# Kernel tuning notes

Measured on AMD Instinct MI355X. Metric: run time of the kernel, lower is better.

Reference implementation:

```python
import jax, jax.numpy as jnp
import numpy as np

WEIGHT = 1.0
TEMPERATURE = 1.0
POWER = 2.0
NEG_FILL = -1e9
EPS = 1e-8


def _cos_sim_matrix(x):
    # row-normalize then GEMM: equivalent to pairwise F.cosine_similarity
    norms = jnp.linalg.norm(x, axis=-1, keepdims=True)
    xn = x / jnp.maximum(norms, EPS)
    return xn @ xn.T  # [N, N]


def setup_inputs() -> dict:
    key = jax.random.key(0)
    k1, k2 = jax.random.split(key)
    model_output = jax.random.normal(k1, (8192, 512), dtype=jnp.float32)
    targets = jax.random.normal(k2, (8192, 768), dtype=jnp.float32)
    return {"model_output": model_output, "targets": targets}


def reference(model_output, targets):
    N = model_output.shape[0]
    eye = jnp.eye(N, dtype=bool)

    sim_o = jnp.where(eye, NEG_FILL, _cos_sim_matrix(model_output))
    sim_t = jnp.where(eye, NEG_FILL, _cos_sim_matrix(targets))

    student_log_probs = jax.nn.log_softmax(sim_o / TEMPERATURE, axis=-1)
    teacher_probs = jax.nn.softmax(sim_t / TEMPERATURE, axis=-1)

    weights = jax.lax.stop_gradient(teacher_probs ** POWER)

    # torch F.kl_div(input=log_p_student, target=p_teacher, reduction='none')
    # = where(target > 0, target * (log(target) - input), 0)
    tp_safe = jnp.where(teacher_probs > 0, teacher_probs, 1.0)
    kl = jnp.where(teacher_probs > 0,
                   teacher_probs * (jnp.log(tp_safe) - student_log_probs),
                   0.0)

    loss = jnp.mean(weights * kl)
    return WEIGHT * loss
```

## Files before the change

kernel.cpp:

```cpp
#include <hip/hip_runtime.h>

#define N    8192
#define DT   768
#define DO   512
#define BM   128
#define BN   128
#define TI   (N / BM)
#define TJ   (N / BN)
#define NTILE (TI * (TI + 1) / 2)
#define NSLOT (2 * TJ)
#define PL    ((size_t)NSLOT * N)
#define NKT   (DT / 32)
#define NKO   (DO / 32)
#define NSTEP (NKT + NKO)

typedef __attribute__((ext_vector_type(8))) short   short8;
typedef __attribute__((ext_vector_type(4))) float   floatx4;

struct alignas(8) us4 { unsigned short x[4]; };

__device__ inline unsigned short f2bf(float x) {
    union { float f; unsigned int u; } v; v.f = x;
    unsigned int r = v.u + 0x7fffu + ((v.u >> 16) & 1u);
    return (unsigned short)(r >> 16);
}
__device__ inline float bf2f(unsigned short u) {
    union { unsigned int u; float f; } v; v.u = ((unsigned int)u) << 16;
    return v.f;
}

__device__ inline void gl2lds16(const unsigned short* g, unsigned short* l) {
    __builtin_amdgcn_global_load_lds(
        (const __attribute__((address_space(1))) unsigned int*)(const void*)g,
        (__attribute__((address_space(3))) unsigned int*)(void*)l,
        16, 0, 0);
}

template <int D>
__device__ inline void stage_tile(const unsigned short* __restrict__ Xi,
                                  const unsigned short* __restrict__ Xj,
                                  unsigned short* sAb, unsigned short* sBb,
                                  int i0, int j0, int k, int t) {
    #pragma unroll
    for (int h = 0; h < 2; ++h) {
        const int idx = t + h * 256;
        const int r   = idx >> 2;
        const int cs  = ((idx & 3) ^ ((r >> 1) & 3)) << 3;
        gl2lds16(Xi + (size_t)(i0 + r) * D + k + cs, &sAb[idx * 8]);
        gl2lds16(Xj + (size_t)(j0 + r) * D + k + cs, &sBb[idx * 8]);
    }
}

__device__ inline void mfma_step(const unsigned short* __restrict__ sAb,
                                 const unsigned short* __restrict__ sBb,
                                 floatx4 (&acc)[4][4],
                                 int wm, int wn, int lr, int lgx) {
    short8 af[4], bf[4];
    #pragma unroll
    for (int mi = 0; mi < 4; ++mi)
        af[mi] = *(const short8*)&sAb[(wm * 64 + mi * 16 + lr) * 32 + (lgx << 3)];
    #pragma unroll
    for (int ni = 0; ni < 4; ++ni)
        bf[ni] = *(const short8*)&sBb[(wn * 64 + ni * 16 + lr) * 32 + (lgx << 3)];
    #pragma unroll
    for (int mi = 0; mi < 4; ++mi)
        #pragma unroll
        for (int ni = 0; ni < 4; ++ni)
            acc[mi][ni] = __builtin_amdgcn_mfma_f32_16x16x32_bf16(
                af[mi], bf[ni], acc[mi][ni], 0, 0, 0);
}

__global__ void norm_kernel(const float* __restrict__ Tg,
                            const float* __restrict__ Mo,
                            unsigned short* __restrict__ Xt,
                            unsigned short* __restrict__ Xo,
                            float* __restrict__ zero_me) {
    if (blockIdx.x == 0 && threadIdx.x == 0) zero_me[0] = 0.0f;
    int bid = blockIdx.x;
    const float* X; unsigned short* Xn; int D;
    if (bid < N / 4) { X = Tg; Xn = Xt; D = DT; }
    else             { bid -= N / 4; X = Mo; Xn = Xo; D = DO; }
    const int row  = bid * 4 + (threadIdx.x >> 6);
    const int lane = threadIdx.x & 63;
    const float* xr = X + (size_t)row * D;
    float ss = 0.0f;
    for (int c = lane * 4; c < D; c += 256) {
        const floatx4 v = *(const floatx4*)(xr + c);
        ss += v[0] * v[0] + v[1] * v[1] + v[2] * v[2] + v[3] * v[3];
    }
    #pragma unroll
    for (int m = 32; m >= 1; m >>= 1) ss += __shfl_xor(ss, m);
    const float scale = 1.0f / fmaxf(sqrtf(ss), 1e-8f);
    unsigned short* outr = Xn + (size_t)row * D;
    for (int c = lane * 4; c < D; c += 256) {
        const floatx4 v = *(const floatx4*)(xr + c);
        us4 o;
        #pragma unroll
        for (int j = 0; j < 4; ++j) o.x[j] = f2bf(v[j] * scale);
        *(us4*)(outr + c) = o;
    }
}

__launch_bounds__(256, 3)
__global__ void fused_kernel(const unsigned short* __restrict__ Xt,
                             const unsigned short* __restrict__ Xo,
                             float* __restrict__ partials,
                             unsigned int* __restrict__ Wws) {
    __shared__ unsigned short sA[3][BM * 32];
    __shared__ unsigned short sB[3][BN * 32];

    const int t    = threadIdx.x;
    const int lane = t & 63;
    const int w    = t >> 6;
    const int wm   = w >> 1, wn = w & 1;
    const int lr   = lane & 15, lg = lane >> 4;
    const int lgx  = lg ^ ((lr >> 1) & 3);

    const int swb = (blockIdx.x & 7) * (NTILE / 8) + (blockIdx.x >> 3);
    int rem = swb, ti = 0;
    while (rem >= TI - ti) { rem -= TI - ti; ++ti; }
    const int tj = ti + rem;
    const bool offdiag = (ti != tj);
    const int i0 = ti * BM, j0 = tj * BN;
    unsigned int* const wt = Wws + (size_t)blockIdx.x * 8192;

    floatx4 acc[4][4];
    #pragma unroll
    for (int a = 0; a < 4; ++a)
        #pragma unroll
        for (int b = 0; b < 4; ++b)
            acc[a][b] = (floatx4){0.0f, 0.0f, 0.0f, 0.0f};

    auto stage_any = [&](int s) {
        unsigned short* a = sA[s % 3];
        unsigned short* b = sB[s % 3];
        if (s < NKT) stage_tile<DT>(Xt, Xt, a, b, i0, j0, s * 32, t);
        else         stage_tile<DO>(Xo, Xo, a, b, i0, j0, (s - NKT) * 32, t);
    };

    stage_any(0);
    stage_any(1);

    for (int kt = 0; kt < NKT; ++kt) {
        stage_any(kt + 2);
        asm volatile("s_waitcnt vmcnt(8)" ::: "memory");
        __builtin_amdgcn_s_barrier();
        asm volatile("" ::: "memory");
        mfma_step(sA[kt % 3], sB[kt % 3], acc, wm, wn, lr, lgx);
        asm volatile("" ::: "memory");
        __builtin_amdgcn_s_barrier();
        asm volatile("" ::: "memory");
    }

    {
        float czt[4], cvv[4], cua[4];
        #pragma unroll
        for (int ni = 0; ni < 4; ++ni) { czt[ni] = 0.0f; cvv[ni] = 0.0f; cua[ni] = 0.0f; }
        #pragma unroll
        for (int mi = 0; mi < 4; ++mi) {
            unsigned int wpk[4][2];
            #pragma unroll
            for (int r = 0; r < 4; ++r) {
                const int row = wm * 64 + mi * 16 + lg * 4 + r;
                const int gi  = i0 + row;
                float zt = 0.0f, vv = 0.0f, ua = 0.0f;
                #pragma unroll
                for (int ni = 0; ni < 4; ++ni) {
                    const int gj = j0 + wn * 64 + ni * 16 + lr;
                    const float a = acc[mi][ni][r];
                    float ea = __expf(a - 1.0f);
                    if (gi == gj) ea = 0.0f;
                    const float e3 = ea * ea * ea;
                    zt += ea; vv += e3; ua += e3 * a;
                    czt[ni] += ea; cvv[ni] += e3; cua[ni] += e3 * a;
                    if ((r & 1) == 0) wpk[ni][r >> 1]  = (unsigned int)f2bf(e3);
                    else              wpk[ni][r >> 1] |= ((unsigned int)f2bf(e3)) << 16;
                }
                #pragma unroll
                for (int m = 8; m >= 1; m >>= 1) {
                    zt += __shfl_xor(zt, m);
                    vv += __shfl_xor(vv, m);
                    ua += __shfl_xor(ua, m);
                }
                if (lr == 0) {
                    const size_t base = (size_t)(tj * 2 + wn) * N + gi;
                    partials[0 * PL + base] = zt;
                    partials[1 * PL + base] = vv;
                    partials[2 * PL + base] = ua;
                }
            }
            #pragma unroll
            for (int ni = 0; ni < 4; ++ni)
                #pragma unroll
                for (int rp = 0; rp < 2; ++rp)
                    wt[(mi * 8 + ni * 2 + rp) * 256 + t] = wpk[ni][rp];
        }
        if (offdiag) {
            #pragma unroll
            for (int ni = 0; ni < 4; ++ni) {
                #pragma unroll
                for (int m = 16; m <= 32; m <<= 1) {
                    czt[ni] += __shfl_xor(czt[ni], m);
                    cvv[ni] += __shfl_xor(cvv[ni], m);
                    cua[ni] += __shfl_xor(cua[ni], m);
                }
            }
            if (lg == 0) {
                #pragma unroll
                for (int ni = 0; ni < 4; ++ni) {
                    const int gj = j0 + wn * 64 + ni * 16 + lr;
                    const size_t base = (size_t)(ti * 2 + wm) * N + gj;
                    partials[0 * PL + base] = czt[ni];
                    partials[1 * PL + base] = cvv[ni];
                    partials[2 * PL + base] = cua[ni];
                }
            }
        }
    }

    #pragma unroll
    for (int a = 0; a < 4; ++a)
        #pragma unroll
        for (int b = 0; b < 4; ++b)
            acc[a][b] = (floatx4){0.0f, 0.0f, 0.0f, 0.0f};

    for (int ko = 0; ko < NKO; ++ko) {
        const int s = NKT + ko;
        if (ko + 2 < NKO) {
            stage_any(s + 2);
            asm volatile("s_waitcnt vmcnt(8)" ::: "memory");
        } else if (ko == NKO - 2) {
            asm volatile("s_waitcnt vmcnt(4)" ::: "memory");
        } else {
            asm volatile("s_waitcnt vmcnt(0)" ::: "memory");
        }
        __builtin_amdgcn_s_barrier();
        asm volatile("" ::: "memory");
        mfma_step(sA[s % 3], sB[s % 3], acc, wm, wn, lr, lgx);
        asm volatile("" ::: "memory");
        if (ko <= NKO - 4) {
            __builtin_amdgcn_s_barrier();
            asm volatile("" ::: "memory");
        }
    }

    {
        unsigned int wld[32];
        #pragma unroll
        for (int pi = 0; pi < 32; ++pi)
            wld[pi] = wt[pi * 256 + t];
        float czo[4], cwb[4];
        #pragma unroll
        for (int ni = 0; ni < 4; ++ni) { czo[ni] = 0.0f; cwb[ni] = 0.0f; }
        #pragma unroll
        for (int mi = 0; mi < 4; ++mi) {
            #pragma unroll
            for (int r = 0; r < 4; ++r) {
                const int row = wm * 64 + mi * 16 + lg * 4 + r;
                const int gi  = i0 + row;
                float zo = 0.0f, wb = 0.0f;
                #pragma unroll
                for (int ni = 0; ni < 4; ++ni) {
                    const int gj = j0 + wn * 64 + ni * 16 + lr;
                    const float b = acc[mi][ni][r];
                    float eb = __expf(b - 1.0f);
                    if (gi == gj) eb = 0.0f;
                    const unsigned int pw = wld[mi * 8 + ni * 2 + (r >> 1)];
                    const float wgt = bf2f((unsigned short)((r & 1) ? (pw >> 16)
                                                                    : (pw & 0xffffu)));
                    zo += eb; wb += wgt * b;
                    czo[ni] += eb; cwb[ni] += wgt * b;
                }
                #pragma unroll
                for (int m = 8; m >= 1; m >>= 1) {
                    zo += __shfl_xor(zo, m);
                    wb += __shfl_xor(wb, m);
                }
                if (lr == 0) {
                    const size_t base = (size_t)(tj * 2 + wn) * N + gi;
                    partials[3 * PL + base] = zo;
                    partials[4 * PL + base] = wb;
                }
            }
        }
        if (offdiag) {
            #pragma unroll
            for (int ni = 0; ni < 4; ++ni) {
                #pragma unroll
                for (int m = 16; m <= 32; m <<= 1) {
                    czo[ni] += __shfl_xor(czo[ni], m);
                    cwb[ni] += __shfl_xor(cwb[ni], m);
                }
            }
            if (lg == 0) {
                #pragma unroll
                for (int ni = 0; ni < 4; ++ni) {
                    const int gj = j0 + wn * 64 + ni * 16 + lr;
                    const size_t base = (size_t)(ti * 2 + wm) * N + gj;
                    partials[3 * PL + base] = czo[ni];
                    partials[4 * PL + base] = cwb[ni];
                }
            }
        }
    }
}

__global__ void reduce_kernel(const float* __restrict__ partials,
                              float* __restrict__ out) {
    __shared__ float sh[5][256];
    const int t    = threadIdx.x;
    const int lane = t & 63;
    const int g    = t >> 6;
    const int i    = blockIdx.x * 64 + lane;
    float s[5] = {0.0f, 0.0f, 0.0f, 0.0f, 0.0f};
    for (int jb = g * (NSLOT / 4); jb < (g + 1) * (NSLOT / 4); ++jb) {
        const size_t base = (size_t)jb * N + i;
        #pragma unroll
        for (int p = 0; p < 5; ++p) s[p] += partials[p * PL + base];
    }
    #pragma unroll
    for (int p = 0; p < 5; ++p) sh[p][t] = s[p];
    __syncthreads();
    if (g == 0) {
        float v[5];
        #pragma unroll
        for (int p = 0; p < 5; ++p)
            v[p] = sh[p][lane] + sh[p][64 + lane] + sh[p][128 + lane] + sh[p][192 + lane];
        float li = (v[2] - v[4] + v[1] * __logf(v[3] / v[0])) / (v[0] * v[0] * v[0]);
        #pragma unroll
        for (int m = 32; m >= 1; m >>= 1) li += __shfl_xor(li, m);
        if (lane == 0)
            atomicAdd(out, li * (1.0f / ((float)N * (float)N)));
    }
}

extern "C" void kernel_launch(void* const* d_in, const int* in_sizes, int n_in,
                              void* d_out, int out_size, void* d_ws, size_t ws_size,
                              hipStream_t stream) {
    (void)in_sizes; (void)n_in; (void)out_size; (void)ws_size;
    const float* mo = (const float*)d_in[0];
    const float* tg = (const float*)d_in[1];
    float* out = (float*)d_out;

    char* ws = (char*)d_ws;
    unsigned short* Xt = (unsigned short*)ws;
    unsigned short* Xo = (unsigned short*)(ws + (size_t)N * DT * 2);
    float* partials    = (float*)(ws + (size_t)N * DT * 2 + (size_t)N * DO * 2);
    unsigned int* Wws  = (unsigned int*)((char*)partials + 5 * PL * sizeof(float));

    norm_kernel<<<2 * (N / 4), 256, 0, stream>>>(tg, mo, Xt, Xo, out);
    fused_kernel<<<NTILE, 256, 0, stream>>>(Xt, Xo, partials, Wws);
    reduce_kernel<<<N / 64, 256, 0, stream>>>(partials, out);
}
```

Baseline: 339.7 us.

## Keep both similarity accumulators in registers and drop weight spill buffer

The fused kernel now holds separate accumulators for the target and output GEMMs and runs a single combined epilogue, so the teacher weights no longer go through a global workspace (bf16 packing, writes and reloads). The K pipeline moves to four LDS stages with one barrier per step, issuing the next load after the barrier. Launch bounds drop from three to two blocks per CU to fit the doubled accumulator registers. The norm kernel caches row values in registers instead of reading each row twice. The trade is lower occupancy against removed global traffic and fewer barriers; the weights now stay in fp32 rather than bf16.

Result: faster. 326.1 us (-4.0%).

```diff
diff --git a/kernel.cpp b/kernel.cpp
--- a/kernel.cpp
+++ b/kernel.cpp
@@ -24,10 +24,6 @@
     unsigned int r = v.u + 0x7fffu + ((v.u >> 16) & 1u);
     return (unsigned short)(r >> 16);
 }
-__device__ inline float bf2f(unsigned short u) {
-    union { unsigned int u; float f; } v; v.u = ((unsigned int)u) << 16;
-    return v.f;
-}
 
 __device__ inline void gl2lds16(const unsigned short* g, unsigned short* l) {
     __builtin_amdgcn_global_load_lds(
@@ -82,32 +78,39 @@
     else             { bid -= N / 4; X = Mo; Xn = Xo; D = DO; }
     const int row  = bid * 4 + (threadIdx.x >> 6);
     const int lane = threadIdx.x & 63;
+    const int nch  = D >> 8;
     const float* xr = X + (size_t)row * D;
+    floatx4 vc[3];
     float ss = 0.0f;
-    for (int c = lane * 4; c < D; c += 256) {
-        const floatx4 v = *(const floatx4*)(xr + c);
-        ss += v[0] * v[0] + v[1] * v[1] + v[2] * v[2] + v[3] * v[3];
+    #pragma unroll
+    for (int h = 0; h < 3; ++h) {
+        if (h < nch) {
+            vc[h] = *(const floatx4*)(xr + lane * 4 + h * 256);
+            ss += vc[h][0] * vc[h][0] + vc[h][1] * vc[h][1]
+                + vc[h][2] * vc[h][2] + vc[h][3] * vc[h][3];
+        }
     }
     #pragma unroll
     for (int m = 32; m >= 1; m >>= 1) ss += __shfl_xor(ss, m);
     const float scale = 1.0f / fmaxf(sqrtf(ss), 1e-8f);
     unsigned short* outr = Xn + (size_t)row * D;
-    for (int c = lane * 4; c < D; c += 256) {
-        const floatx4 v = *(const floatx4*)(xr + c);
-        us4 o;
-        #pragma unroll
-        for (int j = 0; j < 4; ++j) o.x[j] = f2bf(v[j] * scale);
-        *(us4*)(outr + c) = o;
-    }
-}
-
-__launch_bounds__(256, 3)
+    #pragma unroll
+    for (int h = 0; h < 3; ++h) {
+        if (h < nch) {
+            us4 o;
+            #pragma unroll
+            for (int j = 0; j < 4; ++j) o.x[j] = f2bf(vc[h][j] * scale);
+            *(us4*)(outr + lane * 4 + h * 256) = o;
+        }
+    }
+}
+
+__launch_bounds__(256, 2)
 __global__ void fused_kernel(const unsigned short* __restrict__ Xt,
                              const unsigned short* __restrict__ Xo,
-                             float* __restrict__ partials,
-                             unsigned int* __restrict__ Wws) {
-    __shared__ unsigned short sA[3][BM * 32];
-    __shared__ unsigned short sB[3][BN * 32];
+                             float* __restrict__ partials) {
+    __shared__ unsigned short sA[4][BM * 32];
+    __shared__ unsigned short sB[4][BN * 32];
 
     const int t    = threadIdx.x;
     const int lane = t & 63;
@@ -122,78 +125,102 @@
     const int tj = ti + rem;
     const bool offdiag = (ti != tj);
     const int i0 = ti * BM, j0 = tj * BN;
-    unsigned int* const wt = Wws + (size_t)blockIdx.x * 8192;
-
-    floatx4 acc[4][4];
+
+    floatx4 acc_t[4][4], acc_o[4][4];
     #pragma unroll
     for (int a = 0; a < 4; ++a)
         #pragma unroll
-        for (int b = 0; b < 4; ++b)
-            acc[a][b] = (floatx4){0.0f, 0.0f, 0.0f, 0.0f};
+        for (int b = 0; b < 4; ++b) {
+            acc_t[a][b] = (floatx4){0.0f, 0.0f, 0.0f, 0.0f};
+            acc_o[a][b] = (floatx4){0.0f, 0.0f, 0.0f, 0.0f};
+        }
 
     auto stage_any = [&](int s) {
-        unsigned short* a = sA[s % 3];
-        unsigned short* b = sB[s % 3];
+        unsigned short* a = sA[s & 3];
+        unsigned short* b = sB[s & 3];
         if (s < NKT) stage_tile<DT>(Xt, Xt, a, b, i0, j0, s * 32, t);
         else         stage_tile<DO>(Xo, Xo, a, b, i0, j0, (s - NKT) * 32, t);
     };
 
     stage_any(0);
     stage_any(1);
-
-    for (int kt = 0; kt < NKT; ++kt) {
-        stage_any(kt + 2);
+    stage_any(2);
+
+    for (int s = 0; s < NKT; ++s) {
         asm volatile("s_waitcnt vmcnt(8)" ::: "memory");
         __builtin_amdgcn_s_barrier();
         asm volatile("" ::: "memory");
-        mfma_step(sA[kt % 3], sB[kt % 3], acc, wm, wn, lr, lgx);
-        asm volatile("" ::: "memory");
+        stage_any(s + 3);
+        mfma_step(sA[s & 3], sB[s & 3], acc_t, wm, wn, lr, lgx);
+        asm volatile("" ::: "memory");
+    }
+
+    for (int s = NKT; s < NSTEP - 3; ++s) {
+        asm volatile("s_waitcnt vmcnt(8)" ::: "memory");
         __builtin_amdgcn_s_barrier();
         asm volatile("" ::: "memory");
-    }
+        stage_any(s + 3);
+        mfma_step(sA[s & 3], sB[s & 3], acc_o, wm, wn, lr, lgx);
+        asm volatile("" ::: "memory");
+    }
+    asm volatile("s_waitcnt vmcnt(8)" ::: "memory");
+    __builtin_amdgcn_s_barrier();
+    asm volatile("" ::: "memory");
+    mfma_step(sA[37 & 3], sB[37 & 3], acc_o, wm, wn, lr, lgx);
+    asm volatile("s_waitcnt vmcnt(4)" ::: "memory");
+    __builtin_amdgcn_s_barrier();
+    asm volatile("" ::: "memory");
+    mfma_step(sA[38 & 3], sB[38 & 3], acc_o, wm, wn, lr, lgx);
+    asm volatile("s_waitcnt vmcnt(0)" ::: "memory");
+    __builtin_amdgcn_s_barrier();
+    asm volatile("" ::: "memory");
+    mfma_step(sA[39 & 3], sB[39 & 3], acc_o, wm, wn, lr, lgx);
 
     {
-        float czt[4], cvv[4], cua[4];
-        #pragma unroll
-        for (int ni = 0; ni < 4; ++ni) { czt[ni] = 0.0f; cvv[ni] = 0.0f; cua[ni] = 0.0f; }
+        float czt[4], cvv[4], cua[4], czo[4], cwb[4];
+        #pragma unroll
+        for (int ni = 0; ni < 4; ++ni) {
+            czt[ni] = 0.0f; cvv[ni] = 0.0f; cua[ni] = 0.0f;
+            czo[ni] = 0.0f; cwb[ni] = 0.0f;
+        }
         #pragma unroll
         for (int mi = 0; mi < 4; ++mi) {
-            unsigned int wpk[4][2];
             #pragma unroll
             for (int r = 0; r < 4; ++r) {
                 const int row = wm * 64 + mi * 16 + lg * 4 + r;
                 const int gi  = i0 + row;
-                float zt = 0.0f, vv = 0.0f, ua = 0.0f;
+                float zt = 0.0f, vv = 0.0f, ua = 0.0f, zo = 0.0f, wb = 0.0f;
                 #pragma unroll
                 for (int ni = 0; ni < 4; ++ni) {
                     const int gj = j0 + wn * 64 + ni * 16 + lr;
-                    const float a = acc[mi][ni][r];
+                    const float a = acc_t[mi][ni][r];
+                    const float b = acc_o[mi][ni][r];
                     float ea = __expf(a - 1.0f);
-                    if (gi == gj) ea = 0.0f;
+                    float eb = __expf(b - 1.0f);
+                    if (gi == gj) { ea = 0.0f; eb = 0.0f; }
                     const float e3 = ea * ea * ea;
                     zt += ea; vv += e3; ua += e3 * a;
+                    zo += eb; wb += e3 * b;
                     czt[ni] += ea; cvv[ni] += e3; cua[ni] += e3 * a;
-                    if ((r & 1) == 0) wpk[ni][r >> 1]  = (unsigned int)f2bf(e3);
-                    else              wpk[ni][r >> 1] |= ((unsigned int)f2bf(e3)) << 16;
+                    czo[ni] += eb; cwb[ni] += e3 * b;
                 }
                 #pragma unroll
                 for (int m = 8; m >= 1; m >>= 1) {
                     zt += __shfl_xor(zt, m);
                     vv += __shfl_xor(vv, m);
                     ua += __shfl_xor(ua, m);
+                    zo += __shfl_xor(zo, m);
+                    wb += __shfl_xor(wb, m);
                 }
                 if (lr == 0) {
                     const size_t base = (size_t)(tj * 2 + wn) * N + gi;
                     partials[0 * PL + base] = zt;
                     partials[1 * PL + base] = vv;
                     partials[2 * PL + base] = ua;
+                    partials[3 * PL + base] = zo;
+                    partials[4 * PL + base] = wb;
                 }
             }
-            #pragma unroll
-            for (int ni = 0; ni < 4; ++ni)
-                #pragma unroll
-                for (int rp = 0; rp < 2; ++rp)
-                    wt[(mi * 8 + ni * 2 + rp) * 256 + t] = wpk[ni][rp];
         }
         if (offdiag) {
             #pragma unroll
@@ -203,6 +230,8 @@
                     czt[ni] += __shfl_xor(czt[ni], m);
                     cvv[ni] += __shfl_xor(cvv[ni], m);
                     cua[ni] += __shfl_xor(cua[ni], m);
+                    czo[ni] += __shfl_xor(czo[ni], m);
+                    cwb[ni] += __shfl_xor(cwb[ni], m);
                 }
             }
             if (lg == 0) {
@@ -213,90 +242,6 @@
                     partials[0 * PL + base] = czt[ni];
                     partials[1 * PL + base] = cvv[ni];
                     partials[2 * PL + base] = cua[ni];
-                }
-            }
-        }
-    }
-
-    #pragma unroll
-    for (int a = 0; a < 4; ++a)
-        #pragma unroll
-        for (int b = 0; b < 4; ++b)
-            acc[a][b] = (floatx4){0.0f, 0.0f, 0.0f, 0.0f};
-
-    for (int ko = 0; ko < NKO; ++ko) {
-        const int s = NKT + ko;
-        if (ko + 2 < NKO) {
-            stage_any(s + 2);
-            asm volatile("s_waitcnt vmcnt(8)" ::: "memory");
-        } else if (ko == NKO - 2) {
-            asm volatile("s_waitcnt vmcnt(4)" ::: "memory");
-        } else {
-            asm volatile("s_waitcnt vmcnt(0)" ::: "memory");
-        }
-        __builtin_amdgcn_s_barrier();
-        asm volatile("" ::: "memory");
-        mfma_step(sA[s % 3], sB[s % 3], acc, wm, wn, lr, lgx);
-        asm volatile("" ::: "memory");
-        if (ko <= NKO - 4) {
-            __builtin_amdgcn_s_barrier();
-            asm volatile("" ::: "memory");
-        }
-    }
-
-    {
-        unsigned int wld[32];
-        #pragma unroll
-        for (int pi = 0; pi < 32; ++pi)
-            wld[pi] = wt[pi * 256 + t];
-        float czo[4], cwb[4];
-        #pragma unroll
-        for (int ni = 0; ni < 4; ++ni) { czo[ni] = 0.0f; cwb[ni] = 0.0f; }
-        #pragma unroll
-        for (int mi = 0; mi < 4; ++mi) {
-            #pragma unroll
-            for (int r = 0; r < 4; ++r) {
-                const int row = wm * 64 + mi * 16 + lg * 4 + r;
-                const int gi  = i0 + row;
-                float zo = 0.0f, wb = 0.0f;
-                #pragma unroll
-                for (int ni = 0; ni < 4; ++ni) {
-                    const int gj = j0 + wn * 64 + ni * 16 + lr;
-                    const float b = acc[mi][ni][r];
-                    float eb = __expf(b - 1.0f);
-                    if (gi == gj) eb = 0.0f;
-                    const unsigned int pw = wld[mi * 8 + ni * 2 + (r >> 1)];
-                    const float wgt = bf2f((unsigned short)((r & 1) ? (pw >> 16)
-                                                                    : (pw & 0xffffu)));
-                    zo += eb; wb += wgt * b;
-                    czo[ni] += eb; cwb[ni] += wgt * b;
-                }
-                #pragma unroll
-                for (int m = 8; m >= 1; m >>= 1) {
-                    zo += __shfl_xor(zo, m);
-                    wb += __shfl_xor(wb, m);
-                }
-                if (lr == 0) {
-                    const size_t base = (size_t)(tj * 2 + wn) * N + gi;
-                    partials[3 * PL + base] = zo;
-                    partials[4 * PL + base] = wb;
-                }
-            }
-        }
-        if (offdiag) {
-            #pragma unroll
-            for (int ni = 0; ni < 4; ++ni) {
-                #pragma unroll
-                for (int m = 16; m <= 32; m <<= 1) {
-                    czo[ni] += __shfl_xor(czo[ni], m);
-                    cwb[ni] += __shfl_xor(cwb[ni], m);
-                }
-            }
-            if (lg == 0) {
-                #pragma unroll
-                for (int ni = 0; ni < 4; ++ni) {
-                    const int gj = j0 + wn * 64 + ni * 16 + lr;
-                    const size_t base = (size_t)(ti * 2 + wm) * N + gj;
                     partials[3 * PL + base] = czo[ni];
                     partials[4 * PL + base] = cwb[ni];
                 }
@@ -346,9 +291,8 @@
     unsigned short* Xt = (unsigned short*)ws;
     unsigned short* Xo = (unsigned short*)(ws + (size_t)N * DT * 2);
     float* partials    = (float*)(ws + (size_t)N * DT * 2 + (size_t)N * DO * 2);
-    unsigned int* Wws  = (unsigned int*)((char*)partials + 5 * PL * sizeof(float));
 
     norm_kernel<<<2 * (N / 4), 256, 0, stream>>>(tg, mo, Xt, Xo, out);
-    fused_kernel<<<NTILE, 256, 0, stream>>>(Xt, Xo, partials, Wws);
+    fused_kernel<<<NTILE, 256, 0, stream>>>(Xt, Xo, partials);
     reduce_kernel<<<N / 64, 256, 0, stream>>>(partials, out);
 }
```

## Split fused GEMM into teacher and student kernels with single-barrier pipeline

Applied to the files above, without the earlier changes.

Splits the single fused kernel, which ran the teacher GEMM and epilogue then the student GEMM, into two separate kernel launches. Each uses a 3-stage LDS ring with one barrier per k-step, issuing the next prefetch after the barrier instead of before it. The norm kernel now loads each row chunk once into registers rather than reading it twice. The aim is lower register pressure and fewer barriers. The cost is an extra launch and losing overlap between the teacher epilogue and the student loads, with the W workspace round-tripping between the two kernels.

Measured after the change: 325.0 us. 4.3% less time.

```diff
diff --git a/kernel.cpp b/kernel.cpp
--- a/kernel.cpp
+++ b/kernel.cpp
@@ -12,7 +12,6 @@
 #define PL    ((size_t)NSLOT * N)
 #define NKT   (DT / 32)
 #define NKO   (DO / 32)
-#define NSTEP (NKT + NKO)
 
 typedef __attribute__((ext_vector_type(8))) short   short8;
 typedef __attribute__((ext_vector_type(4))) float   floatx4;
@@ -37,8 +36,7 @@
 }
 
 template <int D>
-__device__ inline void stage_tile(const unsigned short* __restrict__ Xi,
-                                  const unsigned short* __restrict__ Xj,
+__device__ inline void stage_tile(const unsigned short* __restrict__ X,
                                   unsigned short* sAb, unsigned short* sBb,
                                   int i0, int j0, int k, int t) {
     #pragma unroll
@@ -46,8 +44,8 @@
         const int idx = t + h * 256;
         const int r   = idx >> 2;
         const int cs  = ((idx & 3) ^ ((r >> 1) & 3)) << 3;
-        gl2lds16(Xi + (size_t)(i0 + r) * D + k + cs, &sAb[idx * 8]);
-        gl2lds16(Xj + (size_t)(j0 + r) * D + k + cs, &sBb[idx * 8]);
+        gl2lds16(X + (size_t)(i0 + r) * D + k + cs, &sAb[idx * 8]);
+        gl2lds16(X + (size_t)(j0 + r) * D + k + cs, &sBb[idx * 8]);
     }
 }
 
@@ -68,6 +66,13 @@
         for (int ni = 0; ni < 4; ++ni)
             acc[mi][ni] = __builtin_amdgcn_mfma_f32_16x16x32_bf16(
                 af[mi], bf[ni], acc[mi][ni], 0, 0, 0);
+}
+
+__device__ inline void tile_coords(int bid, int& ti, int& tj) {
+    const int swb = (bid & 7) * (NTILE / 8) + (bid >> 3);
+    int rem = swb; int a = 0;
+    while (rem >= TI - a) { rem -= TI - a; ++a; }
+    ti = a; tj = a + rem;
 }
 
 __global__ void norm_kernel(const float* __restrict__ Tg,
@@ -82,30 +87,37 @@
     else             { bid -= N / 4; X = Mo; Xn = Xo; D = DO; }
     const int row  = bid * 4 + (threadIdx.x >> 6);
     const int lane = threadIdx.x & 63;
+    const int nch  = D >> 8;
     const float* xr = X + (size_t)row * D;
+    floatx4 vc[3];
     float ss = 0.0f;
-    for (int c = lane * 4; c < D; c += 256) {
-        const floatx4 v = *(const floatx4*)(xr + c);
-        ss += v[0] * v[0] + v[1] * v[1] + v[2] * v[2] + v[3] * v[3];
+    #pragma unroll
+    for (int h = 0; h < 3; ++h) {
+        if (h < nch) {
+            vc[h] = *(const floatx4*)(xr + lane * 4 + h * 256);
+            ss += vc[h][0] * vc[h][0] + vc[h][1] * vc[h][1]
+                + vc[h][2] * vc[h][2] + vc[h][3] * vc[h][3];
+        }
     }
     #pragma unroll
     for (int m = 32; m >= 1; m >>= 1) ss += __shfl_xor(ss, m);
     const float scale = 1.0f / fmaxf(sqrtf(ss), 1e-8f);
     unsigned short* outr = Xn + (size_t)row * D;
-    for (int c = lane * 4; c < D; c += 256) {
-        const floatx4 v = *(const floatx4*)(xr + c);
-        us4 o;
-        #pragma unroll
-        for (int j = 0; j < 4; ++j) o.x[j] = f2bf(v[j] * scale);
-        *(us4*)(outr + c) = o;
+    #pragma unroll
+    for (int h = 0; h < 3; ++h) {
+        if (h < nch) {
+            us4 o;
+            #pragma unroll
+            for (int j = 0; j < 4; ++j) o.x[j] = f2bf(vc[h][j] * scale);
+            *(us4*)(outr + lane * 4 + h * 256) = o;
+        }
     }
 }
 
 __launch_bounds__(256, 3)
-__global__ void fused_kernel(const unsigned short* __restrict__ Xt,
-                             const unsigned short* __restrict__ Xo,
-                             float* __restrict__ partials,
-                             unsigned int* __restrict__ Wws) {
+__global__ void fused_t_kernel(const unsigned short* __restrict__ Xt,
+                               float* __restrict__ partials,
+                               unsigned int* __restrict__ Wws) {
     __shared__ unsigned short sA[3][BM * 32];
     __shared__ unsigned short sB[3][BN * 32];
 
@@ -116,10 +128,7 @@
     const int lr   = lane & 15, lg = lane >> 4;
     const int lgx  = lg ^ ((lr >> 1) & 3);
 
-    const int swb = (blockIdx.x & 7) * (NTILE / 8) + (blockIdx.x >> 3);
-    int rem = swb, ti = 0;
-    while (rem >= TI - ti) { rem -= TI - ti; ++ti; }
-    const int tj = ti + rem;
+    int ti, tj; tile_coords(blockIdx.x, ti, tj);
     const bool offdiag = (ti != tj);
     const int i0 = ti * BM, j0 = tj * BN;
     unsigned int* const wt = Wws + (size_t)blockIdx.x * 8192;
@@ -131,24 +140,17 @@
         for (int b = 0; b < 4; ++b)
             acc[a][b] = (floatx4){0.0f, 0.0f, 0.0f, 0.0f};
 
-    auto stage_any = [&](int s) {
-        unsigned short* a = sA[s % 3];
-        unsigned short* b = sB[s % 3];
-        if (s < NKT) stage_tile<DT>(Xt, Xt, a, b, i0, j0, s * 32, t);
-        else         stage_tile<DO>(Xo, Xo, a, b, i0, j0, (s - NKT) * 32, t);
-    };
-
-    stage_any(0);
-    stage_any(1);
-
-    for (int kt = 0; kt < NKT; ++kt) {
-        stage_any(kt + 2);
-        asm volatile("s_waitcnt vmcnt(8)" ::: "memory");
+    stage_tile<DT>(Xt, sA[0], sB[0], i0, j0, 0, t);
+    stage_tile<DT>(Xt, sA[1], sB[1], i0, j0, 32, t);
+
+    for (int s = 0; s < NKT; ++s) {
+        if (s + 1 < NKT) asm volatile("s_waitcnt vmcnt(4)" ::: "memory");
+        else             asm volatile("s_waitcnt vmcnt(0)" ::: "memory");
         __builtin_amdgcn_s_barrier();
         asm volatile("" ::: "memory");
-        mfma_step(sA[kt % 3], sB[kt % 3], acc, wm, wn, lr, lgx);
-        asm volatile("" ::: "memory");
-        __builtin_amdgcn_s_barrier();
+        if (s + 2 < NKT)
+            stage_tile<DT>(Xt, sA[(s + 2) % 3], sB[(s + 2) % 3], i0, j0, (s + 2) * 32, t);
+        mfma_step(sA[s % 3], sB[s % 3], acc, wm, wn, lr, lgx);
         asm volatile("" ::: "memory");
     }
 
@@ -217,31 +219,46 @@
             }
         }
     }
-
+}
+
+__launch_bounds__(256, 3)
+__global__ void fused_o_kernel(const unsigned short* __restrict__ Xo,
+                               float* __restrict__ partials,
+                               const unsigned int* __restrict__ Wws) {
+    __shared__ unsigned short sA[3][BM * 32];
+    __shared__ unsigned short sB[3][BN * 32];
+
+    const int t    = threadIdx.x;
+    const int lane = t & 63;
+    const int w    = t >> 6;
+    const int wm   = w >> 1, wn = w & 1;
+    const int lr   = lane & 15, lg = lane >> 4;
+    const int lgx  = lg ^ ((lr >> 1) & 3);
+
+    int ti, tj; tile_coords(blockIdx.x, ti, tj);
+    const bool offdiag = (ti != tj);
+    const int i0 = ti * BM, j0 = tj * BN;
+    const unsigned int* const wt = Wws + (size_t)blockIdx.x * 8192;
+
+    floatx4 acc[4][4];
     #pragma unroll
     for (int a = 0; a < 4; ++a)
         #pragma unroll
         for (int b = 0; b < 4; ++b)
             acc[a][b] = (floatx4){0.0f, 0.0f, 0.0f, 0.0f};
 
-    for (int ko = 0; ko < NKO; ++ko) {
-        const int s = NKT + ko;
-        if (ko + 2 < NKO) {
-            stage_any(s + 2);
-            asm volatile("s_waitcnt vmcnt(8)" ::: "memory");
-        } else if (ko == NKO - 2) {
-            asm volatile("s_waitcnt vmcnt(4)" ::: "memory");
-        } else {
-            asm volatile("s_waitcnt vmcnt(0)" ::: "memory");
-        }
+    stage_tile<DO>(Xo, sA[0], sB[0], i0, j0, 0, t);
+    stage_tile<DO>(Xo, sA[1], sB[1], i0, j0, 32, t);
+
+    for (int s = 0; s < NKO; ++s) {
+        if (s + 1 < NKO) asm volatile("s_waitcnt vmcnt(4)" ::: "memory");
+        else             asm volatile("s_waitcnt vmcnt(0)" ::: "memory");
         __builtin_amdgcn_s_barrier();
         asm volatile("" ::: "memory");
+        if (s + 2 < NKO)
+            stage_tile<DO>(Xo, sA[(s + 2) % 3], sB[(s + 2) % 3], i0, j0, (s + 2) * 32, t);
         mfma_step(sA[s % 3], sB[s % 3], acc, wm, wn, lr, lgx);
         asm volatile("" ::: "memory");
-        if (ko <= NKO - 4) {
-            __builtin_amdgcn_s_barrier();
-            asm volatile("" ::: "memory");
-        }
     }
 
     {
@@ -349,6 +366,7 @@
     unsigned int* Wws  = (unsigned int*)((char*)partials + 5 * PL * sizeof(float));
 
     norm_kernel<<<2 * (N / 4), 256, 0, stream>>>(tg, mo, Xt, Xo, out);
-    fused_kernel<<<NTILE, 256, 0, stream>>>(Xt, Xo, partials, Wws);
+    fused_t_kernel<<<NTILE, 256, 0, stream>>>(Xt, partials, Wws);
+    fused_o_kernel<<<NTILE, 256, 0, stream>>>(Xo, partials, Wws);
     reduce_kernel<<<N / 64, 256, 0, stream>>>(partials, out);
 }
```
